# Kernel optimization log

Measured on AMD Instinct MI355X. Metric: run time of the kernel, lower is better.

## Reference

```python
import jax, jax.numpy as jnp
import numpy as np

N = 4096
NFEAT = 512
NHID = 60
NCLASS = 4


def setup_inputs() -> dict:
    key = jax.random.key(0)
    ks = jax.random.split(key, 12)
    x = jax.random.normal(ks[0], (N, NFEAT), dtype=jnp.float32)
    # sparse-ish binary adjacency (sub_adj), symmetric not required by the module
    sub_adj = (jax.random.uniform(ks[1], (N, N)) < 0.002).astype(jnp.float32)
    # P_vec: init to ones (torch.sub in reset_parameters is non-inplace, so it stays ones)
    P_vec = jnp.ones((N * (N + 1) // 2,), dtype=jnp.float32)
    s1 = 1.0 / np.sqrt(NFEAT)
    s2 = 1.0 / np.sqrt(NHID)
    W1 = jax.random.normal(ks[2], (NFEAT, NHID), dtype=jnp.float32) * s1
    b1 = jax.random.normal(ks[3], (NHID,), dtype=jnp.float32) * 0.01
    W2 = jax.random.normal(ks[4], (NHID, NHID), dtype=jnp.float32) * s2
    b2 = jax.random.normal(ks[5], (NHID,), dtype=jnp.float32) * 0.01
    W3 = jax.random.normal(ks[6], (NHID, NHID), dtype=jnp.float32) * s2
    b3 = jax.random.normal(ks[7], (NHID,), dtype=jnp.float32) * 0.01
    lin_w = jax.random.normal(ks[8], (NHID, NCLASS), dtype=jnp.float32) * s2
    lin_b = jax.random.normal(ks[9], (NCLASS,), dtype=jnp.float32) * 0.01
    return {"x": x, "sub_adj": sub_adj, "P_vec": P_vec,
            "W1": W1, "b1": b1, "W2": W2, "b2": b2, "W3": W3, "b3": b3,
            "lin_w": lin_w, "lin_b": lin_b}


def reference(x, sub_adj, P_vec, W1, b1, W2, b2, W3, b3, lin_w, lin_b):
    n = sub_adj.shape[0]
    # scatter P_vec into lower triangle (incl. diagonal), then symmetrize
    il, jl = jnp.tril_indices(n)
    M = jnp.zeros((n, n), dtype=P_vec.dtype).at[il, jl].set(P_vec)
    P_hat_symm = M + M.T - jnp.diag(jnp.diag(M))
    # perturbed adjacency with self-loops
    A_tilde = jax.nn.sigmoid(P_hat_symm) * sub_adj + jnp.eye(n, dtype=P_vec.dtype)
    # degree (column sums, matching python sum(adj)); detached in the original
    d = jax.lax.stop_gradient(jnp.sum(A_tilde, axis=0))
    d_inv_sqrt = jnp.where(d > 0, d ** -0.5, 0.0)  # isinf -> 0
    # D^{-1/2} A D^{-1/2} without materializing diag matrices
    norm_adj = d_inv_sqrt[:, None] * A_tilde * d_inv_sqrt[None, :]
    # 3 GCN layers: spmm(norm_adj, x @ W) + b
    h1 = jax.nn.relu(norm_adj @ (x @ W1) + b1)
    h2 = jax.nn.relu(norm_adj @ (h1 @ W2) + b2)
    h3 = norm_adj @ (h2 @ W3) + b3
    logits = h3 @ lin_w + lin_b  # dropout is identity in eval / p=0
    return jax.nn.log_softmax(logits, axis=1)
```

## Files before the change

### kernel.cpp

```cpp
#include <hip/hip_runtime.h>
#include <math.h>

#define NN 4096
#define NFEAT 512
#define NHID 60
#define NCLASS 4
#define CAP 96
#define GSTRIDE 64
#define XW_BLKS (NN / 4)
#define SCAN_BLKS 2048
#define SCAN_THREADS (SCAN_BLKS * 256)

__global__ __launch_bounds__(256) void k_scan_xw(const float* __restrict__ adj,
                                                 const float* __restrict__ P,
                                                 float* __restrict__ dcol,
                                                 int* __restrict__ cnt,
                                                 int* __restrict__ cols,
                                                 float* __restrict__ vals,
                                                 const float* __restrict__ x,
                                                 const float* __restrict__ W1,
                                                 float* __restrict__ g1) {
    if (blockIdx.x >= XW_BLKS) {
        const int t = (blockIdx.x - XW_BLKS) * 256 + threadIdx.x;
        const float4* adj4 = (const float4*)adj;
        float4 a[8];
        #pragma unroll
        for (int m = 0; m < 8; ++m)
            a[m] = adj4[m * SCAN_THREADS + t];
        #pragma unroll
        for (int m = 0; m < 8; ++m) {
            const float4 v = a[m];
            if (v.x + v.y + v.z + v.w == 0.f) continue;
            const float av[4] = {v.x, v.y, v.z, v.w};
            const int e0 = (m * SCAN_THREADS + t) * 4;
            #pragma unroll
            for (int q = 0; q < 4; ++q) {
                if (av[q] != 0.f) {
                    const int e = e0 + q;
                    const int i = e >> 12;
                    const int j = e & (NN - 1);
                    const int hi = i > j ? i : j;
                    const int lo = i > j ? j : i;
                    const float pv = P[((hi * (hi + 1)) >> 1) + lo];
                    const float s = av[q] / (1.f + __expf(-pv));
                    atomicAdd(&dcol[j], s);
                    const int pos = atomicAdd(&cnt[i], 1);
                    if (pos < CAP) { cols[i * CAP + pos] = j; vals[i * CAP + pos] = s; }
                }
            }
        }
    } else {
        __shared__ float part[1024];
        const int tid = threadIdx.x;
        const int w = tid >> 6, lane = tid & 63;
        const int c = lane < NHID ? lane : 0;
        const int row0 = blockIdx.x * 4;
        const int k0 = w * (NFEAT / 4);
        const float* x0 = x + (row0 + 0) * NFEAT;
        const float* x1 = x + (row0 + 1) * NFEAT;
        const float* x2 = x + (row0 + 2) * NFEAT;
        const float* x3 = x + (row0 + 3) * NFEAT;
        float a0 = 0.f, a1 = 0.f, a2 = 0.f, a3 = 0.f;
        for (int k = k0; k < k0 + NFEAT / 4; k += 4) {
            const float4 xv0 = *(const float4*)(x0 + k);
            const float4 xv1 = *(const float4*)(x1 + k);
            const float4 xv2 = *(const float4*)(x2 + k);
            const float4 xv3 = *(const float4*)(x3 + k);
            const float w0 = W1[(k + 0) * NHID + c];
            const float w1 = W1[(k + 1) * NHID + c];
            const float w2 = W1[(k + 2) * NHID + c];
            const float w3 = W1[(k + 3) * NHID + c];
            a0 = fmaf(xv0.x, w0, fmaf(xv0.y, w1, fmaf(xv0.z, w2, fmaf(xv0.w, w3, a0))));
            a1 = fmaf(xv1.x, w0, fmaf(xv1.y, w1, fmaf(xv1.z, w2, fmaf(xv1.w, w3, a1))));
            a2 = fmaf(xv2.x, w0, fmaf(xv2.y, w1, fmaf(xv2.z, w2, fmaf(xv2.w, w3, a2))));
            a3 = fmaf(xv3.x, w0, fmaf(xv3.y, w1, fmaf(xv3.z, w2, fmaf(xv3.w, w3, a3))));
        }
        part[(w * 4 + 0) * 64 + lane] = a0;
        part[(w * 4 + 1) * 64 + lane] = a1;
        part[(w * 4 + 2) * 64 + lane] = a2;
        part[(w * 4 + 3) * 64 + lane] = a3;
        __syncthreads();
        const float o = part[(0 * 4 + w) * 64 + lane] + part[(1 * 4 + w) * 64 + lane]
                      + part[(2 * 4 + w) * 64 + lane] + part[(3 * 4 + w) * 64 + lane];
        g1[(row0 + w) * GSTRIDE + lane] = (lane < NHID) ? o : 0.f;
    }
}

__device__ __forceinline__ float spmm_row(const float* __restrict__ gin,
                                          const float* __restrict__ dcol,
                                          const int* __restrict__ cnt,
                                          const int* __restrict__ cols,
                                          const float* __restrict__ vals,
                                          int i, int lane, float di) {
    const int nn = min(cnt[i], CAP);
    float acc = gin[i * GSTRIDE + lane] * di;
    const int4*   c4 = (const int4*)(cols + i * CAP);
    const float4* v4 = (const float4*)(vals + i * CAP);
    int e = 0;
    for (; e + 4 <= nn; e += 4) {
        const int4   jj = c4[e >> 2];
        const float4 vv = v4[e >> 2];
        const float f0 = vv.x * rsqrtf(1.f + dcol[jj.x]);
        const float f1 = vv.y * rsqrtf(1.f + dcol[jj.y]);
        const float f2 = vv.z * rsqrtf(1.f + dcol[jj.z]);
        const float f3 = vv.w * rsqrtf(1.f + dcol[jj.w]);
        const float g0 = gin[jj.x * GSTRIDE + lane];
        const float g1 = gin[jj.y * GSTRIDE + lane];
        const float g2 = gin[jj.z * GSTRIDE + lane];
        const float g3 = gin[jj.w * GSTRIDE + lane];
        acc = fmaf(f0, g0, fmaf(f1, g1, fmaf(f2, g2, fmaf(f3, g3, acc))));
    }
    for (; e < nn; ++e) {
        const int j = cols[i * CAP + e];
        const float f = vals[i * CAP + e] * rsqrtf(1.f + dcol[j]);
        acc = fmaf(f, gin[j * GSTRIDE + lane], acc);
    }
    return acc * di;
}

__global__ __launch_bounds__(256) void k_layer(const float* __restrict__ gin,
                                               float* __restrict__ gout,
                                               const float* __restrict__ dcol,
                                               const int* __restrict__ cnt,
                                               const int* __restrict__ cols,
                                               const float* __restrict__ vals,
                                               const float* __restrict__ bias,
                                               const float* __restrict__ W) {
    __shared__ float hs[256];
    const int w = threadIdx.x >> 6, lane = threadIdx.x & 63;
    const int i = blockIdx.x * 4 + w;
    const float di = rsqrtf(1.f + dcol[i]);
    const float acc = spmm_row(gin, dcol, cnt, cols, vals, i, lane, di);
    float hv = 0.f;
    if (lane < NHID) hv = fmaxf(acc + bias[lane], 0.f);
    hs[w * 64 + lane] = hv;
    const int c = lane < NHID ? lane : 0;
    float o = 0.f;
    #pragma unroll 4
    for (int k = 0; k < NHID; ++k)
        o = fmaf(hs[w * 64 + k], W[k * NHID + c], o);
    gout[i * GSTRIDE + lane] = (lane < NHID) ? o : 0.f;
}

__global__ __launch_bounds__(256) void k_final(const float* __restrict__ gin,
                                               float* __restrict__ out,
                                               const float* __restrict__ dcol,
                                               const int* __restrict__ cnt,
                                               const int* __restrict__ cols,
                                               const float* __restrict__ vals,
                                               const float* __restrict__ b3,
                                               const float* __restrict__ lw,
                                               const float* __restrict__ lb) {
    __shared__ float hs[256];
    const int w = threadIdx.x >> 6, lane = threadIdx.x & 63;
    const int i = blockIdx.x * 4 + w;
    const float di = rsqrtf(1.f + dcol[i]);
    const float acc = spmm_row(gin, dcol, cnt, cols, vals, i, lane, di);
    hs[w * 64 + lane] = (lane < NHID) ? acc + b3[lane] : 0.f;
    if (lane < NCLASS) {
        float o = lb[lane];
        #pragma unroll 4
        for (int k = 0; k < NHID; ++k)
            o = fmaf(hs[w * 64 + k], lw[k * NCLASS + lane], o);
        float m = fmaxf(o, __shfl_xor(o, 1));
        m = fmaxf(m, __shfl_xor(m, 2));
        const float ex = __expf(o - m);
        float ss = ex + __shfl_xor(ex, 1);
        ss += __shfl_xor(ss, 2);
        out[i * NCLASS + lane] = o - m - __logf(ss);
    }
}

extern "C" void kernel_launch(void* const* d_in, const int* in_sizes, int n_in,
                              void* d_out, int out_size, void* d_ws, size_t ws_size,
                              hipStream_t stream) {
    const float* x   = (const float*)d_in[0];
    const float* adj = (const float*)d_in[1];
    const float* P   = (const float*)d_in[2];
    const float* W1  = (const float*)d_in[3];
    const float* b1  = (const float*)d_in[4];
    const float* W2  = (const float*)d_in[5];
    const float* b2  = (const float*)d_in[6];
    const float* W3  = (const float*)d_in[7];
    const float* b3  = (const float*)d_in[8];
    const float* lw  = (const float*)d_in[9];
    const float* lb  = (const float*)d_in[10];
    float* out = (float*)d_out;

    char* ws = (char*)d_ws;
    float* dcol = (float*)(ws);
    int*   cnt  = (int*)(ws + 16384);
    int*   cols = (int*)(ws + 32768);
    float* vals = (float*)(ws + 32768 + 1572864);
    float* bufA = (float*)(ws + 32768 + 2 * 1572864);
    float* bufB = (float*)(ws + 32768 + 2 * 1572864 + 1048576);

    hipMemsetAsync(ws, 0, 32768, stream);

    k_scan_xw<<<XW_BLKS + SCAN_BLKS, 256, 0, stream>>>(adj, P, dcol, cnt, cols, vals,
                                                       x, W1, bufA);
    k_layer<<<NN / 4, 256, 0, stream>>>(bufA, bufB, dcol, cnt, cols, vals, b1, W2);
    k_layer<<<NN / 4, 256, 0, stream>>>(bufB, bufA, dcol, cnt, cols, vals, b2, W3);
    k_final<<<NN / 4, 256, 0, stream>>>(bufA, out, dcol, cnt, cols, vals, b3, lw, lb);
}
```

Baseline: 195.4 us.

## Split adjacency scan into compaction pass and separate edge-processing kernel

```diff
diff --git a/kernel.cpp b/kernel.cpp
--- a/kernel.cpp
+++ b/kernel.cpp
@@ -7,47 +7,68 @@
 #define NCLASS 4
 #define CAP 96
 #define GSTRIDE 64
-#define XW_BLKS (NN / 4)
 #define SCAN_BLKS 2048
 #define SCAN_THREADS (SCAN_BLKS * 256)
-
-__global__ __launch_bounds__(256) void k_scan_xw(const float* __restrict__ adj,
-                                                 const float* __restrict__ P,
-                                                 float* __restrict__ dcol,
-                                                 int* __restrict__ cnt,
-                                                 int* __restrict__ cols,
-                                                 float* __restrict__ vals,
-                                                 const float* __restrict__ x,
-                                                 const float* __restrict__ W1,
-                                                 float* __restrict__ g1) {
-    if (blockIdx.x >= XW_BLKS) {
-        const int t = (blockIdx.x - XW_BLKS) * 256 + threadIdx.x;
-        const float4* adj4 = (const float4*)adj;
-        float4 a[8];
-        #pragma unroll
-        for (int m = 0; m < 8; ++m)
-            a[m] = adj4[m * SCAN_THREADS + t];
-        #pragma unroll
-        for (int m = 0; m < 8; ++m) {
-            const float4 v = a[m];
-            if (v.x + v.y + v.z + v.w == 0.f) continue;
-            const float av[4] = {v.x, v.y, v.z, v.w};
-            const int e0 = (m * SCAN_THREADS + t) * 4;
+#define LQ_CAP 512
+#define XW_BLKS (NN / 4)
+#define EDGE_BLKS 256
+
+__global__ __launch_bounds__(256) void k_scan(const float* __restrict__ adj,
+                                              int* __restrict__ qn,
+                                              int* __restrict__ equeue) {
+    __shared__ int lq[LQ_CAP];
+    __shared__ int lcnt, gbase;
+    if (threadIdx.x == 0) lcnt = 0;
+    __syncthreads();
+    const int t = blockIdx.x * 256 + threadIdx.x;
+    const float4* adj4 = (const float4*)adj;
+    #pragma unroll
+    for (int m = 0; m < 8; ++m) {
+        const int v = m * SCAN_THREADS + t;
+        const float4 a = adj4[v];
+        if (a.x + a.y + a.z + a.w != 0.f) {
+            const float av[4] = {a.x, a.y, a.z, a.w};
             #pragma unroll
             for (int q = 0; q < 4; ++q) {
                 if (av[q] != 0.f) {
-                    const int e = e0 + q;
-                    const int i = e >> 12;
-                    const int j = e & (NN - 1);
-                    const int hi = i > j ? i : j;
-                    const int lo = i > j ? j : i;
-                    const float pv = P[((hi * (hi + 1)) >> 1) + lo];
-                    const float s = av[q] / (1.f + __expf(-pv));
-                    atomicAdd(&dcol[j], s);
-                    const int pos = atomicAdd(&cnt[i], 1);
-                    if (pos < CAP) { cols[i * CAP + pos] = j; vals[i * CAP + pos] = s; }
+                    const int pos = atomicAdd(&lcnt, 1);
+                    if (pos < LQ_CAP) lq[pos] = v * 4 + q;
                 }
             }
+        }
+    }
+    __syncthreads();
+    if (threadIdx.x == 0) gbase = atomicAdd(qn, lcnt);
+    __syncthreads();
+    const int n = min(lcnt, LQ_CAP);
+    for (int k = threadIdx.x; k < n; k += 256)
+        equeue[gbase + k] = lq[k];
+}
+
+__global__ __launch_bounds__(256) void k_edges_xw(const float* __restrict__ P,
+                                                  const int* __restrict__ qn,
+                                                  const int* __restrict__ equeue,
+                                                  float* __restrict__ dcol,
+                                                  int* __restrict__ cnt,
+                                                  int* __restrict__ cols,
+                                                  float* __restrict__ vals,
+                                                  const float* __restrict__ x,
+                                                  const float* __restrict__ W1,
+                                                  float* __restrict__ g1) {
+    if (blockIdx.x >= XW_BLKS) {
+        const int gtid = (blockIdx.x - XW_BLKS) * 256 + threadIdx.x;
+        const int total = qn[0];
+        for (int idx = gtid; idx < total; idx += EDGE_BLKS * 256) {
+            const int e = equeue[idx];
+            const int i = e >> 12;
+            const int j = e & (NN - 1);
+            const int hi = i > j ? i : j;
+            const int lo = i > j ? j : i;
+            const float pv = P[((hi * (hi + 1)) >> 1) + lo];
+            const float s = 1.f / (1.f + __expf(-pv));
+            atomicAdd(&dcol[j], s);
+            const int pos = atomicAdd(&cnt[i], 1);
+            if (pos < CAP) { cols[i * CAP + pos] = j; vals[i * CAP + pos] = s; }
         }
     } else {
         __shared__ float part[1024];
@@ -188,17 +209,20 @@
     float* out = (float*)d_out;
 
     char* ws = (char*)d_ws;
-    float* dcol = (float*)(ws);
-    int*   cnt  = (int*)(ws + 16384);
-    int*   cols = (int*)(ws + 32768);
-    float* vals = (float*)(ws + 32768 + 1572864);
-    float* bufA = (float*)(ws + 32768 + 2 * 1572864);
-    float* bufB = (float*)(ws + 32768 + 2 * 1572864 + 1048576);
-
-    hipMemsetAsync(ws, 0, 32768, stream);
-
-    k_scan_xw<<<XW_BLKS + SCAN_BLKS, 256, 0, stream>>>(adj, P, dcol, cnt, cols, vals,
-                                                       x, W1, bufA);
+    float* dcol   = (float*)(ws);
+    int*   cnt    = (int*)(ws + 16384);
+    int*   qn     = (int*)(ws + 32768);
+    int*   equeue = (int*)(ws + 36864);
+    int*   cols   = (int*)(ws + 36864 + 1048576);
+    float* vals   = (float*)(ws + 36864 + 1048576 + 1572864);
+    float* bufA   = (float*)(ws + 36864 + 1048576 + 2 * 1572864);
+    float* bufB   = (float*)(ws + 36864 + 1048576 + 2 * 1572864 + 1048576);
+
+    hipMemsetAsync(ws, 0, 36864, stream);
+
+    k_scan    <<<SCAN_BLKS, 256, 0, stream>>>(adj, qn, equeue);
+    k_edges_xw<<<XW_BLKS + EDGE_BLKS, 256, 0, stream>>>(P, qn, equeue, dcol, cnt,
+                                                        cols, vals, x, W1, bufA);
     k_layer<<<NN / 4, 256, 0, stream>>>(bufA, bufB, dcol, cnt, cols, vals, b1, W2);
     k_layer<<<NN / 4, 256, 0, stream>>>(bufB, bufA, dcol, cnt, cols, vals, b2, W3);
     k_final<<<NN / 4, 256, 0, stream>>>(bufA, out, dcol, cnt, cols, vals, b3, lw, lb);
```

Result: slower. 206.3 us (+5.6%).
